# Optimization experiments

Hardware: AMD Instinct MI355X
Metric: run time of the kernel (lower is better)

The kernel has to match this reference:

```python
import jax, jax.numpy as jnp
import numpy as np

N_NODES = 50000
NUM_FEA = 213
HID, IN_HEAD = 16, 12
OUT_DIM, OUT_HEAD = 8, 8
NEG_SLOPE = 0.2


def gat_conv(x, W, att_src, att_dst, bias, src, dst, H, C):
    # x: [N, F] -> h: [N, H, C]
    N = x.shape[0]
    h = (x @ W).reshape(N, H, C)
    a_s = jnp.sum(h * att_src, axis=-1)  # [N, H]
    a_d = jnp.sum(h * att_dst, axis=-1)  # [N, H]
    e = jax.nn.leaky_relu(a_s[src] + a_d[dst], NEG_SLOPE)  # [E, H]
    # segment softmax over incoming edges of each dst node
    m = jax.ops.segment_max(e, dst, num_segments=N)
    ex = jnp.exp(e - m[dst])
    denom = jax.ops.segment_sum(ex, dst, num_segments=N)
    alpha = ex / denom[dst]  # [E, H]
    out = jax.ops.segment_sum(h[src] * alpha[:, :, None], dst, num_segments=N)
    return out.reshape(N, H * C) + bias


def setup_inputs() -> dict:
    key = jax.random.key(0)
    ks = jax.random.split(key, 16)
    E = 800000
    P = 16384
    features = jax.random.normal(ks[0], (N_NODES, NUM_FEA), dtype=jnp.float32)
    edge_index = jax.random.randint(ks[1], (2, E), 0, N_NODES, dtype=jnp.int32)
    node1_index = jax.random.randint(ks[2], (P,), 0, N_NODES, dtype=jnp.int32)
    node2_index = jax.random.randint(ks[3], (P,), 0, N_NODES, dtype=jnp.int32)
    s1 = 1.0 / np.sqrt(NUM_FEA)
    s2 = 1.0 / np.sqrt(HID * IN_HEAD)
    s3 = 1.0 / np.sqrt(OUT_DIM * OUT_HEAD * 2)
    params = {
        'W1': jax.random.normal(ks[4], (NUM_FEA, IN_HEAD * HID), jnp.float32) * s1,
        'att_src1': jax.random.normal(ks[5], (IN_HEAD, HID), jnp.float32) * s1,
        'att_dst1': jax.random.normal(ks[6], (IN_HEAD, HID), jnp.float32) * s1,
        'b1': jnp.zeros((IN_HEAD * HID,), jnp.float32),
        'W2': jax.random.normal(ks[7], (IN_HEAD * HID, OUT_HEAD * OUT_DIM), jnp.float32) * s2,
        'att_src2': jax.random.normal(ks[8], (OUT_HEAD, OUT_DIM), jnp.float32) * s2,
        'att_dst2': jax.random.normal(ks[9], (OUT_HEAD, OUT_DIM), jnp.float32) * s2,
        'b2': jnp.zeros((OUT_HEAD * OUT_DIM,), jnp.float32),
        'linW': jax.random.normal(ks[10], (OUT_DIM * OUT_HEAD * 2, 2), jnp.float32) * s3,
        'linb': jnp.zeros((2,), jnp.float32),
    }
    return dict(features=features, edge_index=edge_index,
                node1_index=node1_index, node2_index=node2_index, **params)


def reference(features, edge_index, node1_index, node2_index,
              W1, att_src1, att_dst1, b1, W2, att_src2, att_dst2, b2, linW, linb):
    # eval mode: dropout(p=0.8) is identity
    N = features.shape[0]
    self_loops = jnp.arange(N, dtype=edge_index.dtype)
    src = jnp.concatenate([edge_index[0], self_loops])
    dst = jnp.concatenate([edge_index[1], self_loops])
    x = gat_conv(features, W1, att_src1, att_dst1, b1, src, dst, IN_HEAD, HID)
    x = jax.nn.elu(x)
    x = gat_conv(x, W2, att_src2, att_dst2, b2, src, dst, OUT_HEAD, OUT_DIM)
    x = jax.nn.elu(x)
    pair = jnp.concatenate([x[node1_index], x[node2_index]], axis=1)
    y_pred = jax.nn.sigmoid(pair @ linW + linb)
    return (y_pred, x)
```

## Files before the change

### kernel.cpp

```cpp
#include <hip/hip_runtime.h>
#include <hip/hip_bf16.h>

#define HID1 16
#define NHEAD1 12
#define F1 (HID1*NHEAD1)
#define HID2 8
#define NHEAD2 8
#define F2 (HID2*NHEAD2)
#define NUM_FEA 213
#define NEG_SLOPE 0.2f
#define KP 224
#define KP2 192
#define LDK 40
#define MR1 64
#define MR2 64
#define NC1 224
#define NW2R 80
#define SLOTS 56
#define BINS 256
#define NPB 196
#define CAP 4096
#define FILLB 256
#define EPT 13

typedef __attribute__((ext_vector_type(8))) __bf16 bf16x8;
typedef __attribute__((ext_vector_type(4))) float floatx4;
typedef __attribute__((ext_vector_type(2))) float floatx2;
typedef float floatx4u __attribute__((ext_vector_type(4), aligned(4)));
typedef unsigned short ushort_t;

static __device__ __forceinline__ unsigned short f2bf(float f) {
    unsigned u = __float_as_uint(f);
    unsigned r = (u + 0x7fffu + ((u >> 16) & 1u)) >> 16;
    return (unsigned short)r;
}
static __device__ __forceinline__ float lrelu(float e) {
    return e > 0.f ? e : NEG_SLOPE * e;
}
static __device__ __forceinline__ float elu(float v) {
    return v > 0.f ? v : (__expf(v) - 1.f);
}


__global__ __launch_bounds__(256) void wprep_kernel(
        const float* __restrict__ W1, const float* __restrict__ as1w,
        const float* __restrict__ ad1w, ushort_t* __restrict__ Wt1,
        const float* __restrict__ W2, const float* __restrict__ as2w,
        const float* __restrict__ ad2w, ushort_t* __restrict__ Wt2) {
    int j = blockIdx.x * 256 + threadIdx.x;
    if (j < NC1 * KP) {
        int n = j / KP, k = j - n * KP;
        float v = 0.f;
        if (k < NUM_FEA) {
            if (n < 192) {
                v = W1[(long)k * F1 + n];
            } else if (n < 204) {
                int hd = n - 192;
                for (int c = 0; c < HID1; c++)
                    v += W1[(long)k * F1 + hd * HID1 + c] * as1w[hd * HID1 + c];
            } else if (n < 216) {
                int hd = n - 204;
                for (int c = 0; c < HID1; c++)
                    v += W1[(long)k * F1 + hd * HID1 + c] * ad1w[hd * HID1 + c];
            }
        }
        Wt1[j] = f2bf(v);
    } else {
        int j2 = j - NC1 * KP;
        if (j2 < NW2R * KP2) {
            int n = j2 / KP2, k = j2 - n * KP2;
            float v;
            if (n < 64) {
                v = W2[(long)k * F2 + n];
            } else if (n < 72) {
                int hd = n - 64;
                v = 0.f;
                for (int c = 0; c < HID2; c++)
                    v += W2[(long)k * F2 + hd * HID2 + c] * as2w[hd * HID2 + c];
            } else {
                int hd = n - 72;
                v = 0.f;
                for (int c = 0; c < HID2; c++)
                    v += W2[(long)k * F2 + hd * HID2 + c] * ad2w[hd * HID2 + c];
            }
            Wt2[j2] = f2bf(v);
        }
    }
}


static __device__ __forceinline__ void stageA(ushort_t* dst, const float* xp,
                                              bool ok, int col) {
    union { int4 q; ushort_t u[8]; } pk;
    if (ok && col + 8 <= NUM_FEA) {
        floatx4u a = *(const floatx4u*)(xp + col);
        floatx4u c = *(const floatx4u*)(xp + col + 4);
#pragma unroll
        for (int j = 0; j < 4; j++) { pk.u[j] = f2bf(a[j]); pk.u[4 + j] = f2bf(c[j]); }
    } else {
#pragma unroll
        for (int j = 0; j < 8; j++) {
            float v = (ok && col + j < NUM_FEA) ? xp[col + j] : 0.f;
            pk.u[j] = f2bf(v);
        }
    }
    *(int4*)dst = pk.q;
}

__global__ __launch_bounds__(256) void gemm1_fill_kernel(
        const float* __restrict__ X, const ushort_t* __restrict__ Wt,
        ushort_t* __restrict__ Hout, float* __restrict__ as_, float* __restrict__ ad_,
        const int* __restrict__ ei, int* __restrict__ binctr,
        unsigned* __restrict__ binbuf, int E, int Etot,
        int N, int nblk_gemm) {
    __shared__ ushort_t As[MR1 * LDK];
    __shared__ ushort_t Bs[NC1 * LDK];
    __shared__ int hist[BINS];
    __shared__ int cur[BINS];
    int tid = threadIdx.x;
    if ((int)blockIdx.x >= nblk_gemm) {
        int fb = (int)blockIdx.x - nblk_gemm;
        if (tid < BINS) hist[tid] = 0;
        __syncthreads();
        unsigned stash[EPT];
        int base_e = fb * 256 + tid;
#pragma unroll
        for (int i = 0; i < EPT; i++) {
            int e = base_e + i * (FILLB * 256);
            unsigned pk = 0xffffffffu;
            if (e < Etot) {
                int s, d;
                if (e < E) { s = ei[e]; d = ei[E + e]; } else { s = e - E; d = s; }
                pk = (unsigned)s | ((unsigned)d << 16);
                atomicAdd(&hist[(unsigned)d / NPB], 1);
            }
            stash[i] = pk;
        }
        __syncthreads();
        if (tid < BINS) cur[tid] = atomicAdd(&binctr[tid], hist[tid]);
        __syncthreads();
#pragma unroll
        for (int i = 0; i < EPT; i++) {
            unsigned pk = stash[i];
            if (pk != 0xffffffffu) {
                int d = (int)(pk >> 16);
                int bin = (int)((unsigned)d / NPB);
                int dl = d - bin * NPB;
                int r = atomicAdd(&cur[bin], 1);
                if (r < CAP)
                    binbuf[(long)bin * CAP + r] = (pk & 0xffffu) | ((unsigned)dl << 16);
            }
        }
        return;
    }
    int wave = tid >> 6, lane = tid & 63;
    int q = lane >> 4, l16 = lane & 15;
    int wm = (wave >> 1) * 32;
    int wn = (wave & 1) * 112;
    long row0 = (long)blockIdx.x * MR1;

    int r0 = tid >> 2, ksl = (tid & 3) * 8;
    long gr0 = row0 + r0;
    bool ok0 = gr0 < N;
    const float* xp0 = X + gr0 * NUM_FEA;
    ushort_t* lds0 = &As[r0 * LDK + ksl];

    floatx4 acc[2][7] = {};

    for (int k0 = 0; k0 < KP; k0 += 32) {
        stageA(lds0, xp0, ok0, k0 + ksl);
#pragma unroll
        for (int p = 0; p < 4; p++) {
            int idx = p * 256 + tid;
            if (idx < NC1 * 4) {
                int r = idx >> 2, ks = (idx & 3) * 8;
                *(int4*)&Bs[r * LDK + ks] = *(const int4*)&Wt[(long)r * KP + k0 + ks];
            }
        }
        __syncthreads();
        bf16x8 af[2], bfr[7];
#pragma unroll
        for (int rt = 0; rt < 2; rt++)
            af[rt] = *(const bf16x8*)&As[(wm + rt * 16 + l16) * LDK + q * 8];
#pragma unroll
        for (int ct = 0; ct < 7; ct++)
            bfr[ct] = *(const bf16x8*)&Bs[(wn + ct * 16 + l16) * LDK + q * 8];
#pragma unroll
        for (int rt = 0; rt < 2; rt++)
#pragma unroll
            for (int ct = 0; ct < 7; ct++)
                acc[rt][ct] = __builtin_amdgcn_mfma_f32_16x16x32_bf16(af[rt], bfr[ct], acc[rt][ct], 0, 0, 0);
        __syncthreads();
    }
#pragma unroll
    for (int rt = 0; rt < 2; rt++) {
#pragma unroll
        for (int r = 0; r < 4; r++) {
            long grow = row0 + wm + rt * 16 + q * 4 + r;
            if (grow < N) {
#pragma unroll
                for (int ct = 0; ct < 7; ct++) {
                    int col = wn + ct * 16 + l16;
                    float v = acc[rt][ct][r];
                    if (col < 192)      Hout[grow * F1 + col] = f2bf(v);
                    else if (col < 204) as_[grow * NHEAD1 + col - 192] = v;
                    else if (col < 216) ad_[grow * NHEAD1 + col - 204] = v;
                }
            }
        }
    }
}


__global__ __launch_bounds__(256) void binsort_kernel(
        const unsigned* __restrict__ binbuf, const int* __restrict__ binctr,
        ushort_t* __restrict__ esrcp, int* __restrict__ cnt, int N) {
    __shared__ int lcnt[NPB];
    int b = blockIdx.x, tid = threadIdx.x;
    if (tid < NPB) lcnt[tid] = 0;
    __syncthreads();
    int cntb = binctr[b];
    if (cntb > CAP) cntb = CAP;
    const unsigned* seg = binbuf + (long)b * CAP;
    for (int t = tid; t < cntb; t += 256) {
        unsigned u = seg[t];
        int s = (int)(u & 0xffffu);
        int dl = (int)(u >> 16);
        int slot = atomicAdd(&lcnt[dl], 1);
        if (slot < SLOTS)
            esrcp[(long)(b * NPB + dl) * SLOTS + slot] = (ushort_t)s;
    }
    __syncthreads();
    int d = b * NPB + tid;
    if (tid < NPB && d < N) cnt[d] = lcnt[tid];
}


__global__ __launch_bounds__(256) void gemm2_mfma(const ushort_t* __restrict__ Xbf,
                                                  const ushort_t* __restrict__ Wt,
                                                  ushort_t* __restrict__ Hout,
                                                  float* __restrict__ as_,
                                                  float* __restrict__ ad_, int N) {
    __shared__ ushort_t As[MR2 * LDK];
    __shared__ ushort_t Bs[96 * LDK];
    int tid = threadIdx.x;
    int wave = tid >> 6, lane = tid & 63;
    int q = lane >> 4, l16 = lane & 15;
    int wm = (wave >> 1) * 32;
    int wn = (wave & 1) * 48;
    long row0 = (long)blockIdx.x * MR2;

    int r0 = tid >> 2, ksl = (tid & 3) * 8;

    floatx4 acc[2][3] = {};

    for (int k0 = 0; k0 < KP2; k0 += 32) {
        *(int4*)&As[r0 * LDK + ksl] = *(const int4*)&Xbf[(row0 + r0) * KP2 + k0 + ksl];
#pragma unroll
        for (int p = 0; p < 2; p++) {
            int idx = p * 256 + tid;
            if (idx < 96 * 4) {
                int r = idx >> 2, ks = (idx & 3) * 8;
                int4 z = {0, 0, 0, 0};
                *(int4*)&Bs[r * LDK + ks] = (r < NW2R) ? *(const int4*)&Wt[(long)r * KP2 + k0 + ks] : z;
            }
        }
        __syncthreads();
        bf16x8 af[2], bfr[3];
#pragma unroll
        for (int rt = 0; rt < 2; rt++)
            af[rt] = *(const bf16x8*)&As[(wm + rt * 16 + l16) * LDK + q * 8];
#pragma unroll
        for (int ct = 0; ct < 3; ct++)
            bfr[ct] = *(const bf16x8*)&Bs[(wn + ct * 16 + l16) * LDK + q * 8];
#pragma unroll
        for (int rt = 0; rt < 2; rt++)
#pragma unroll
            for (int ct = 0; ct < 3; ct++)
                acc[rt][ct] = __builtin_amdgcn_mfma_f32_16x16x32_bf16(af[rt], bfr[ct], acc[rt][ct], 0, 0, 0);
        __syncthreads();
    }
#pragma unroll
    for (int rt = 0; rt < 2; rt++) {
#pragma unroll
        for (int r = 0; r < 4; r++) {
            long grow = row0 + wm + rt * 16 + q * 4 + r;
            if (grow < N) {
#pragma unroll
                for (int ct = 0; ct < 3; ct++) {
                    int col = wn + ct * 16 + l16;
                    float v = acc[rt][ct][r];
                    if (col < 64)      Hout[grow * F2 + col] = f2bf(v);
                    else if (col < 72) as_[grow * NHEAD2 + col - 64] = v;
                    else if (col < 80) ad_[grow * NHEAD2 + col - 72] = v;
                }
            }
        }
    }
}


__global__ __launch_bounds__(256) void gather1_kernel(const int* __restrict__ cnt,
                                                      const ushort_t* __restrict__ esrcp,
                                                      const float* __restrict__ as_,
                                                      const float* __restrict__ ad_,
                                                      const ushort_t* __restrict__ h,
                                                      const float* __restrict__ bias,
                                                      ushort_t* __restrict__ xout, int N) {
    int d = blockIdx.x * 4 + (threadIdx.x >> 6);
    if (d >= N) return;
    int l = threadIdx.x & 63;
    int jc = l < 48 ? l : 47;
    int hj = jc >> 2;
    int e0 = l / 12, h0 = l - e0 * 12;
    int l64 = l + 64;
    int e1 = l64 / 12, h1 = l64 - e1 * 12;
    int deg = cnt[d]; if (deg > SLOTS) deg = SLOTS;
    int sfull = (int)esrcp[d * SLOTS + (l < SLOTS - 1 ? l : SLOTS - 1)];
    float adv0 = ad_[d * NHEAD1 + h0];
    float adv1 = ad_[d * NHEAD1 + h1];
    float4 b4 = ((const float4*)bias)[jc];
    const char* hcol = (const char*)(h + 4 * jc);

    floatx2 a01 = {0.f, 0.f}, a23 = {0.f, 0.f};
    float accd = 0.f;

    for (int p0 = 0; p0 < deg; p0 += 8) {
        int s_e[8];
#pragma unroll
        for (int i = 0; i < 8; i++) s_e[i] = __shfl(sfull, p0 + i, 64);
        uint2 g[8];
#pragma unroll
        for (int i = 0; i < 8; i++) {
            unsigned off = (unsigned)s_e[i] * (unsigned)(F1 * 2);
            g[i] = *(const uint2*)(hcol + off);
        }
        int sq0 = __shfl(sfull, p0 + e0, 64);
        int sq1 = __shfl(sfull, p0 + e1, 64);
        float a0v = as_[sq0 * NHEAD1 + h0];
        float a1v = as_[sq1 * NHEAD1 + h1];
        float w0 = (p0 + e0 < deg) ? __expf(lrelu(a0v + adv0)) : 0.f;
        float w1 = (e1 < 8 && p0 + e1 < deg) ? __expf(lrelu(a1v + adv1)) : 0.f;
#pragma unroll
        for (int i = 0; i < 8; i++) {
            float wi;
            if (i <= 4) {
                wi = __shfl(w0, i * 12 + hj, 64);
            } else if (i == 5) {
                float wa = __shfl(w0, 60 + hj, 64);
                int srcb = hj >= 4 ? hj - 4 : 0;
                float wb = __shfl(w1, srcb, 64);
                wi = (hj < 4) ? wa : wb;
            } else {
                wi = __shfl(w1, i * 12 + hj - 64, 64);
            }
            unsigned x = g[i].x, y = g[i].y;
            floatx2 h01, h23, w2;
            h01.x = __uint_as_float(x << 16);
            h01.y = __uint_as_float(x & 0xffff0000u);
            h23.x = __uint_as_float(y << 16);
            h23.y = __uint_as_float(y & 0xffff0000u);
            w2.x = wi; w2.y = wi;
            a01 += w2 * h01;
            a23 += w2 * h23;
            accd += wi;
        }
    }
    if (l < 48) {
        float inv = __builtin_amdgcn_rcpf(accd);
        float v0 = elu(a01.x * inv + b4.x);
        float v1 = elu(a01.y * inv + b4.y);
        float v2 = elu(a23.x * inv + b4.z);
        float v3 = elu(a23.y * inv + b4.w);
        uint2 outp;
        outp.x = (unsigned)f2bf(v0) | ((unsigned)f2bf(v1) << 16);
        outp.y = (unsigned)f2bf(v2) | ((unsigned)f2bf(v3) << 16);
        *(uint2*)(xout + (long)d * F1 + 4 * l) = outp;
    }
}


__global__ __launch_bounds__(256) void gather2_kernel(const int* __restrict__ cnt,
                                                      const ushort_t* __restrict__ esrcp,
                                                      const float* __restrict__ as_,
                                                      const float* __restrict__ ad_,
                                                      const ushort_t* __restrict__ h,
                                                      const float* __restrict__ bias,
                                                      float* __restrict__ xout, int N) {
    int d = blockIdx.x * 4 + (threadIdx.x >> 6);
    if (d >= N) return;
    int l = threadIdx.x & 63;
    int cg = l & 15;
    int hj = cg >> 1;
    int e_lo = l >> 4;
    int ie0 = l >> 3, hq = l & 7;
    int ie1 = 8 + ie0;
    int deg = cnt[d]; if (deg > SLOTS) deg = SLOTS;
    int sfull = (int)esrcp[d * SLOTS + (l < SLOTS - 1 ? l : SLOTS - 1)];
    float advq = ad_[d * NHEAD2 + hq];
    const char* hcol = (const char*)(h + 4 * cg);

    floatx2 a01 = {0.f, 0.f}, a23 = {0.f, 0.f};
    float accd = 0.f;

    for (int p0 = 0; p0 < deg; p0 += 16) {
        int se[4];
#pragma unroll
        for (int k = 0; k < 4; k++) se[k] = __shfl(sfull, p0 + e_lo + 4 * k, 64);
        uint2 g[4];
#pragma unroll
        for (int k = 0; k < 4; k++) {
            unsigned off = (unsigned)se[k] * (unsigned)(F2 * 2);
            g[k] = *(const uint2*)(hcol + off);
        }
        int sq0 = __shfl(sfull, p0 + ie0, 64);
        int sq1 = __shfl(sfull, p0 + ie1, 64);
        float a0v = as_[sq0 * NHEAD2 + hq];
        float a1v = as_[sq1 * NHEAD2 + hq];
        float w0d = (p0 + ie0 < deg) ? __expf(lrelu(a0v + advq)) : 0.f;
        float w1d = (p0 + ie1 < deg) ? __expf(lrelu(a1v + advq)) : 0.f;
#pragma unroll
        for (int k = 0; k < 4; k++) {
            int i = e_lo + 4 * k;
            float wk = (k < 2) ? __shfl(w0d, i * 8 + hj, 64)
                               : __shfl(w1d, i * 8 + hj - 64, 64);
            unsigned x = g[k].x, y = g[k].y;
            floatx2 h01, h23, w2;
            h01.x = __uint_as_float(x << 16);
            h01.y = __uint_as_float(x & 0xffff0000u);
            h23.x = __uint_as_float(y << 16);
            h23.y = __uint_as_float(y & 0xffff0000u);
            w2.x = wk; w2.y = wk;
            a01 += w2 * h01;
            a23 += w2 * h23;
            accd += wk;
        }
    }
    a01.x += __shfl_xor(a01.x, 16, 64); a01.x += __shfl_xor(a01.x, 32, 64);
    a01.y += __shfl_xor(a01.y, 16, 64); a01.y += __shfl_xor(a01.y, 32, 64);
    a23.x += __shfl_xor(a23.x, 16, 64); a23.x += __shfl_xor(a23.x, 32, 64);
    a23.y += __shfl_xor(a23.y, 16, 64); a23.y += __shfl_xor(a23.y, 32, 64);
    accd  += __shfl_xor(accd, 16, 64);  accd  += __shfl_xor(accd, 32, 64);
    if (l < 16) {
        float4 b4 = ((const float4*)bias)[cg];
        float inv = __builtin_amdgcn_rcpf(accd);
        float4 outp;
        outp.x = elu(a01.x * inv + b4.x);
        outp.y = elu(a01.y * inv + b4.y);
        outp.z = elu(a23.x * inv + b4.z);
        outp.w = elu(a23.y * inv + b4.w);
        *(float4*)(xout + (long)d * F2 + 4 * cg) = outp;
    }
}


__global__ void pair_kernel(const float* __restrict__ x, const int* __restrict__ n1,
                            const int* __restrict__ n2, const float* __restrict__ linW,
                            const float* __restrict__ linb, float* __restrict__ y, int P) {
    int idx = blockIdx.x * blockDim.x + threadIdx.x;
    if (idx >= P) return;
    const float4* xa = (const float4*)(x + (long)n1[idx] * F2);
    const float4* xb = (const float4*)(x + (long)n2[idx] * F2);
    float a0 = linb[0], a1 = linb[1];
#pragma unroll
    for (int k4 = 0; k4 < F2 / 4; k4++) {
        float4 v = xa[k4];
        int k = k4 * 4;
        a0 += v.x * linW[2 * k] + v.y * linW[2 * (k + 1)] + v.z * linW[2 * (k + 2)] + v.w * linW[2 * (k + 3)];
        a1 += v.x * linW[2 * k + 1] + v.y * linW[2 * (k + 1) + 1] + v.z * linW[2 * (k + 2) + 1] + v.w * linW[2 * (k + 3) + 1];
    }
#pragma unroll
    for (int k4 = 0; k4 < F2 / 4; k4++) {
        float4 v = xb[k4];
        int k = F2 + k4 * 4;
        a0 += v.x * linW[2 * k] + v.y * linW[2 * (k + 1)] + v.z * linW[2 * (k + 2)] + v.w * linW[2 * (k + 3)];
        a1 += v.x * linW[2 * k + 1] + v.y * linW[2 * (k + 1) + 1] + v.z * linW[2 * (k + 2) + 1] + v.w * linW[2 * (k + 3) + 1];
    }
    y[2 * idx]     = 1.f / (1.f + __expf(-a0));
    y[2 * idx + 1] = 1.f / (1.f + __expf(-a1));
}


extern "C" void kernel_launch(void* const* d_in, const int* in_sizes, int n_in,
                              void* d_out, int out_size, void* d_ws, size_t ws_size,
                              hipStream_t stream) {
    const float* features = (const float*)d_in[0];
    const int*   ei       = (const int*)d_in[1];
    const int*   n1       = (const int*)d_in[2];
    const int*   n2       = (const int*)d_in[3];
    const float* W1       = (const float*)d_in[4];
    const float* att_s1   = (const float*)d_in[5];
    const float* att_d1   = (const float*)d_in[6];
    const float* b1       = (const float*)d_in[7];
    const float* W2       = (const float*)d_in[8];
    const float* att_s2   = (const float*)d_in[9];
    const float* att_d2   = (const float*)d_in[10];
    const float* b2       = (const float*)d_in[11];
    const float* linW     = (const float*)d_in[12];
    const float* linb     = (const float*)d_in[13];

    const int N = in_sizes[0] / NUM_FEA;
    const int E = in_sizes[1] / 2;
    const int P = in_sizes[2];
    const int Etot = E + N;

    const int nblk1 = (N + MR1 - 1) / MR1;
    const int nblk2 = (N + MR2 - 1) / MR2;
    const int nwb = (NC1 * KP + NW2R * KP2 + 255) / 256;

    float* ws = (float*)d_ws;
    long o = 0;
    float* h1r  = ws + o; o += (long)N * F1 / 2;
    float* x1r  = ws + o; o += (long)N * F1 / 2;
    float* as1  = ws + o; o += (long)N * NHEAD1;
    float* ad1  = ws + o; o += (long)N * NHEAD1;
    float* h2r  = ws + o; o += (long)N * F2 / 2;
    float* as2  = ws + o; o += (long)N * NHEAD2;
    float* ad2  = ws + o; o += (long)N * NHEAD2;
    float* w1r  = ws + o; o += ((long)NC1 * KP + 1) / 2;
    float* w2r  = ws + o; o += ((long)NW2R * KP2 + 1) / 2;
    float* esr  = ws + o; o += ((long)N * SLOTS + 1) / 2;
    unsigned* binbuf = (unsigned*)(ws + o); o += (long)BINS * CAP;
    int* binctr = (int*)(ws + o); o += BINS;
    int* cnt  = (int*)(ws + o); o += N;

    ushort_t* h1b   = (ushort_t*)h1r;
    ushort_t* x1bf  = (ushort_t*)x1r;
    ushort_t* h2b   = (ushort_t*)h2r;
    ushort_t* Wt1   = (ushort_t*)w1r;
    ushort_t* Wt2   = (ushort_t*)w2r;
    ushort_t* esrcp = (ushort_t*)esr;

    float* y_out = (float*)d_out;
    float* x_out = (float*)d_out + (long)2 * P;

    hipMemsetAsync(binctr, 0, (size_t)BINS * sizeof(int), stream);

    wprep_kernel<<<nwb, 256, 0, stream>>>(W1, att_s1, att_d1, Wt1,
                                          W2, att_s2, att_d2, Wt2);

    gemm1_fill_kernel<<<nblk1 + FILLB, 256, 0, stream>>>(
        features, Wt1, h1b, as1, ad1, ei, binctr, binbuf, E, Etot, N, nblk1);

    binsort_kernel<<<BINS, 256, 0, stream>>>(binbuf, binctr, esrcp, cnt, N);

    gather1_kernel<<<(N + 3) / 4, 256, 0, stream>>>(cnt, esrcp, as1, ad1, h1b, b1, x1bf, N);

    gemm2_mfma<<<nblk2, 256, 0, stream>>>(x1bf, Wt2, h2b, as2, ad2, N);
    gather2_kernel<<<(N + 3) / 4, 256, 0, stream>>>(cnt, esrcp, as2, ad2, h2b, b2, x_out, N);

    pair_kernel<<<(P + 255) / 256, 256, 0, stream>>>(x_out, n1, n2, linW, linb, y_out, P);
}
```

Baseline: 249.1 us.

## Stage binsort rows in LDS, sort sources per node, and fold memset into wprep

The binsort kernel now builds each bin's per-node source slot rows in shared memory and then writes them to global memory with coalesced int4 stores, replacing scattered 2-byte global writes. Each node's source list is insertion-sorted so the later gather kernels read neighbor rows in ascending order, which may improve locality. The bin-counter memset is folded into wprep_kernel, removing a separate launch. The costs are about 22KB of LDS per block, a serial per-thread sort, and a slightly larger esrcp buffer because whole bins are now written.

```diff
diff --git a/kernel.cpp b/kernel.cpp
--- a/kernel.cpp
+++ b/kernel.cpp
@@ -46,7 +46,9 @@
         const float* __restrict__ W1, const float* __restrict__ as1w,
         const float* __restrict__ ad1w, ushort_t* __restrict__ Wt1,
         const float* __restrict__ W2, const float* __restrict__ as2w,
-        const float* __restrict__ ad2w, ushort_t* __restrict__ Wt2) {
+        const float* __restrict__ ad2w, ushort_t* __restrict__ Wt2,
+        int* __restrict__ binctr) {
+    if (blockIdx.x == 0 && threadIdx.x < BINS) binctr[threadIdx.x] = 0;
     int j = blockIdx.x * 256 + threadIdx.x;
     if (j < NC1 * KP) {
         int n = j / KP, k = j - n * KP;
@@ -215,9 +217,15 @@
 __global__ __launch_bounds__(256) void binsort_kernel(
         const unsigned* __restrict__ binbuf, const int* __restrict__ binctr,
         ushort_t* __restrict__ esrcp, int* __restrict__ cnt, int N) {
+    __shared__ ushort_t rows[NPB * SLOTS];
     __shared__ int lcnt[NPB];
     int b = blockIdx.x, tid = threadIdx.x;
     if (tid < NPB) lcnt[tid] = 0;
+    {
+        int4 z = {0, 0, 0, 0};
+        int4* rz = (int4*)rows;
+        for (int t = tid; t < NPB * SLOTS / 8; t += 256) rz[t] = z;
+    }
     __syncthreads();
     int cntb = binctr[b];
     if (cntb > CAP) cntb = CAP;
@@ -228,11 +236,25 @@
         int dl = (int)(u >> 16);
         int slot = atomicAdd(&lcnt[dl], 1);
         if (slot < SLOTS)
-            esrcp[(long)(b * NPB + dl) * SLOTS + slot] = (ushort_t)s;
+            rows[dl * SLOTS + slot] = (ushort_t)s;
     }
     __syncthreads();
-    int d = b * NPB + tid;
-    if (tid < NPB && d < N) cnt[d] = lcnt[tid];
+    if (tid < NPB) {
+        int dg = lcnt[tid]; if (dg > SLOTS) dg = SLOTS;
+        ushort_t* r = &rows[tid * SLOTS];
+        for (int i = 1; i < dg; i++) {
+            ushort_t key = r[i];
+            int j = i - 1;
+            while (j >= 0 && r[j] > key) { r[j + 1] = r[j]; j--; }
+            r[j + 1] = key;
+        }
+        int d = b * NPB + tid;
+        if (d < N) cnt[d] = lcnt[tid];
+    }
+    __syncthreads();
+    int4* dst = (int4*)(esrcp + (long)b * NPB * SLOTS);
+    const int4* src = (const int4*)rows;
+    for (int t = tid; t < NPB * SLOTS / 8; t += 256) dst[t] = src[t];
 }
 
 
@@ -519,7 +541,7 @@
     float* ad2  = ws + o; o += (long)N * NHEAD2;
     float* w1r  = ws + o; o += ((long)NC1 * KP + 1) / 2;
     float* w2r  = ws + o; o += ((long)NW2R * KP2 + 1) / 2;
-    float* esr  = ws + o; o += ((long)N * SLOTS + 1) / 2;
+    float* esr  = ws + o; o += ((long)BINS * NPB * SLOTS + 1) / 2;
     unsigned* binbuf = (unsigned*)(ws + o); o += (long)BINS * CAP;
     int* binctr = (int*)(ws + o); o += BINS;
     int* cnt  = (int*)(ws + o); o += N;
@@ -534,10 +556,8 @@
     float* y_out = (float*)d_out;
     float* x_out = (float*)d_out + (long)2 * P;
 
-    hipMemsetAsync(binctr, 0, (size_t)BINS * sizeof(int), stream);
-
     wprep_kernel<<<nwb, 256, 0, stream>>>(W1, att_s1, att_d1, Wt1,
-                                          W2, att_s2, att_d2, Wt2);
+                                          W2, att_s2, att_d2, Wt2, binctr);
 
     gemm1_fill_kernel<<<nblk1 + FILLB, 256, 0, stream>>>(
         features, Wt1, h1b, as1, ad1, ei, binctr, binbuf, E, Etot, N, nblk1);
```

Result: slower. 292.4 us (+17.4%).
